# Optimization experiments

Hardware: AMD Instinct MI355X
Metric: run time of the kernel (lower is better)

Reference implementation:

```python
import jax, jax.numpy as jnp
import numpy as np

STRIDE = 16
A = 9
PRE_NMS_TOP_N = 6000
POST_NMS_TOP_N = 300
NMS_THRESH = 0.7
MIN_SIZE = 16
H, W = 128, 192


def _generate_anchors(base_size=16, ratios=(0.5, 1.0, 2.0), scales=(8, 16, 32)):
    base = np.array([0, 0, base_size - 1, base_size - 1], dtype=np.float64)
    w = base[2] - base[0] + 1
    h = base[3] - base[1] + 1
    x_ctr = base[0] + 0.5 * (w - 1)
    y_ctr = base[1] + 0.5 * (h - 1)
    size = w * h
    ratios = np.array(ratios)
    ws = np.round(np.sqrt(size / ratios))
    hs = np.round(ws * ratios)
    ratio_anchors = np.stack([x_ctr - 0.5 * (ws - 1), y_ctr - 0.5 * (hs - 1),
                              x_ctr + 0.5 * (ws - 1), y_ctr + 0.5 * (hs - 1)], axis=1)
    out = []
    scales = np.array(scales)
    for a in ratio_anchors:
        aw = a[2] - a[0] + 1
        ah = a[3] - a[1] + 1
        xc = a[0] + 0.5 * (aw - 1)
        yc = a[1] + 0.5 * (ah - 1)
        ws2 = aw * scales
        hs2 = ah * scales
        out.append(np.stack([xc - 0.5 * (ws2 - 1), yc - 0.5 * (hs2 - 1),
                             xc + 0.5 * (ws2 - 1), yc + 0.5 * (hs2 - 1)], axis=1))
    return np.concatenate(out, axis=0).astype(np.float32)  # [9,4]


def setup_inputs() -> dict:
    key = jax.random.key(0)
    k1, k2 = jax.random.split(key)
    scores = jax.random.uniform(k1, (1, 2 * A, H, W), dtype=jnp.float32)
    bbox_deltas = 0.1 * jax.random.normal(k2, (1, 4 * A, H, W), dtype=jnp.float32)
    im_info = jnp.array([[H * STRIDE, W * STRIDE, 1.0]], dtype=jnp.float32)
    return {"scores": scores, "bbox_deltas": bbox_deltas, "im_info": im_info}


def _proposal_forward(scores, bbox_deltas, im_info):
    anchors_base = jnp.asarray(_generate_anchors())  # [A,4]
    sc = scores[:, A:, :, :]                          # fg scores [1,A,H,W]
    h, w = sc.shape[-2], sc.shape[-1]
    shift_x = (jnp.arange(w) * STRIDE).astype(sc.dtype)
    shift_y = (jnp.arange(h) * STRIDE).astype(sc.dtype)
    sy, sx = jnp.meshgrid(shift_y, shift_x, indexing='ij')
    shifts = jnp.stack([sx.ravel(), sy.ravel(), sx.ravel(), sy.ravel()], axis=1)  # [K,4]
    anchors = (anchors_base[None, :, :] + shifts[:, None, :]).reshape(-1, 4)      # [K*A,4]

    deltas = bbox_deltas.transpose(0, 2, 3, 1).reshape(-1, 4)
    deltas = jnp.concatenate([deltas[:, :2], jnp.clip(deltas[:, 2:], -10.0, 10.0)], axis=1)
    sc = sc.transpose(0, 2, 3, 1).reshape(-1)  # [K*A]

    widths = anchors[:, 2] - anchors[:, 0] + 1.0
    heights = anchors[:, 3] - anchors[:, 1] + 1.0
    ctr_x = anchors[:, 0] + 0.5 * widths
    ctr_y = anchors[:, 1] + 0.5 * heights
    dx, dy, dw, dh = deltas[:, 0], deltas[:, 1], deltas[:, 2], deltas[:, 3]
    pcx = dx * widths + ctr_x
    pcy = dy * heights + ctr_y
    pw = jnp.exp(dw) * widths
    ph = jnp.exp(dh) * heights
    x1 = pcx - 0.5 * pw
    y1 = pcy - 0.5 * ph
    x2 = pcx + 0.5 * pw
    y2 = pcy + 0.5 * ph

    info = im_info[0]
    x1 = jnp.clip(x1, 0.0, info[1] - 1.0)
    x2 = jnp.clip(x2, 0.0, info[1] - 1.0)
    y1 = jnp.clip(y1, 0.0, info[0] - 1.0)
    y2 = jnp.clip(y2, 0.0, info[0] - 1.0)
    proposals = jnp.stack([x1, y1, x2, y2], axis=1)

    # filter_boxes: mask (instead of dropping) boxes smaller than min_size*scale
    min_sz = MIN_SIZE * info[2]
    valid = ((x2 - x1 + 1.0) >= min_sz) & ((y2 - y1 + 1.0) >= min_sz)
    masked = jnp.where(valid, sc, -jnp.inf)

    # sort desc + pre_nms_topN
    top_scores, top_idx = jax.lax.top_k(masked, PRE_NMS_TOP_N)
    boxes = proposals[top_idx]               # [PRE,4], score-descending
    tvalid = top_scores > -jnp.inf

    # pairwise IoU (torchvision convention)
    area = (boxes[:, 2] - boxes[:, 0]) * (boxes[:, 3] - boxes[:, 1])
    lt = jnp.maximum(boxes[:, None, :2], boxes[None, :, :2])
    rb = jnp.minimum(boxes[:, None, 2:], boxes[None, :, 2:])
    wh = jnp.clip(rb - lt, 0.0)
    inter = wh[..., 0] * wh[..., 1]
    iou = inter / (area[:, None] + area[None, :] - inter)  # [PRE,PRE]

    # greedy NMS over score-sorted boxes
    n = PRE_NMS_TOP_N
    def step(keep, x):
        iou_col, v, i = x
        suppressed = jnp.any(keep & (iou_col > NMS_THRESH))
        k = v & jnp.logical_not(suppressed)
        keep = keep.at[i].set(k)
        return keep, k
    keep, _ = jax.lax.scan(step, jnp.zeros((n,), dtype=bool),
                           (iou.T, tvalid, jnp.arange(n)))

    # kept boxes first (stable => score order preserved), take post_nms_topN
    order = jnp.argsort(jnp.logical_not(keep).astype(jnp.int32), stable=True)[:POST_NMS_TOP_N]
    kept = keep[order]
    out_boxes = jnp.where(kept[:, None], boxes[order], 0.0)
    output = jnp.concatenate(
        [jnp.zeros((POST_NMS_TOP_N, 1), out_boxes.dtype), out_boxes], axis=1)
    return output  # [POST,5]: (batch_idx=0, x1,y1,x2,y2); rows beyond kept count are zero


def reference(scores, bbox_deltas, im_info):
    return _proposal_forward(scores, bbox_deltas, im_info)
```

## Files before the change

kernel.cpp:

```cpp
#include <hip/hip_runtime.h>

#define N_ANCH 221184
#define HW     24576
#define Wd     192
#define AA     9
#define TOPN   6000
#define POSTN  300
#define NWORDS 94
#define NCHUNK 47
#define GRID   512
#define GSTRIDE (GRID * 256)
#define SEGSZ  1024
#define CAND_CAP 8192

typedef unsigned long long u64;
typedef unsigned int u32;

__device__ const float c_aw[9] = {184.f,368.f,736.f,128.f,256.f,512.f, 88.f,176.f,352.f};
__device__ const float c_ah[9] = { 96.f,192.f,384.f,128.f,256.f,512.f,176.f,352.f,704.f};

__device__ __forceinline__ u32 ald32(const u32* p) {
    return __hip_atomic_load((const u32*)p, __ATOMIC_RELAXED, __HIP_MEMORY_SCOPE_AGENT);
}
__device__ __forceinline__ void ast32(u32* p, u32 v) {
    __hip_atomic_store(p, v, __ATOMIC_RELAXED, __HIP_MEMORY_SCOPE_AGENT);
}
__device__ __forceinline__ u64 ald64(const u64* p) {
    return __hip_atomic_load((const u64*)p, __ATOMIC_RELAXED, __HIP_MEMORY_SCOPE_AGENT);
}
__device__ __forceinline__ void ast64(u64* p, u64 v) {
    __hip_atomic_store(p, v, __ATOMIC_RELAXED, __HIP_MEMORY_SCOPE_AGENT);
}
__device__ __forceinline__ void stf4(float4* p, float4 v) {
    u64 lo, hi;
    float2 a = make_float2(v.x, v.y), b = make_float2(v.z, v.w);
    __builtin_memcpy(&lo, &a, 8); __builtin_memcpy(&hi, &b, 8);
    ast64((u64*)p, lo); ast64(((u64*)p) + 1, hi);
}
__device__ __forceinline__ float4 ldf4(const float4* p) {
    u64 lo = ald64((const u64*)p), hi = ald64(((const u64*)p) + 1);
    float2 a, b;
    __builtin_memcpy(&a, &lo, 8); __builtin_memcpy(&b, &hi, 8);
    return make_float4(a.x, a.y, b.x, b.y);
}

__device__ __forceinline__ void gbar(u32* bar, u32 target) {
    __syncthreads();
    if (threadIdx.x == 0) {
        __hip_atomic_fetch_add(bar, 1u, __ATOMIC_RELAXED, __HIP_MEMORY_SCOPE_AGENT);
        int guard = 0;
        while (__hip_atomic_load(bar, __ATOMIC_RELAXED, __HIP_MEMORY_SCOPE_AGENT) < target) {
            __builtin_amdgcn_s_sleep(1);
            if (++guard > (1 << 22)) break;
        }
    }
    __syncthreads();
}

__device__ __forceinline__ float4 decode_box(int a, int cell,
                                             const float* __restrict__ deltas,
                                             float info0, float info1, float info2,
                                             bool* valid) {
    int h = cell / Wd;
    int w = cell - h * Wd;
    const float* db = deltas + (size_t)(4 * a) * HW + cell;
    float dx = db[0];
    float dy = db[HW];
    float dw = db[2 * HW];
    float dh = db[3 * HW];
    dw = fminf(fmaxf(dw, -10.f), 10.f);
    dh = fminf(fmaxf(dh, -10.f), 10.f);

    float ww = c_aw[a], hh = c_ah[a];
    float cx = 16.f * (float)w + 8.f;
    float cy = 16.f * (float)h + 8.f;

    float pcx = __fadd_rn(__fmul_rn(dx, ww), cx);
    float pcy = __fadd_rn(__fmul_rn(dy, hh), cy);
    float pw  = __fmul_rn(expf(dw), ww);
    float ph  = __fmul_rn(expf(dh), hh);
    float hpw = __fmul_rn(0.5f, pw);
    float hph = __fmul_rn(0.5f, ph);
    float x1 = __fsub_rn(pcx, hpw);
    float x2 = __fadd_rn(pcx, hpw);
    float y1 = __fsub_rn(pcy, hph);
    float y2 = __fadd_rn(pcy, hph);

    float xmax = __fsub_rn(info1, 1.f);
    float ymax = __fsub_rn(info0, 1.f);
    x1 = fminf(fmaxf(x1, 0.f), xmax);
    x2 = fminf(fmaxf(x2, 0.f), xmax);
    y1 = fminf(fmaxf(y1, 0.f), ymax);
    y2 = fminf(fmaxf(y2, 0.f), ymax);

    float msz = __fmul_rn(16.f, info2);
    *valid = (__fadd_rn(__fsub_rn(x2, x1), 1.f) >= msz) &&
             (__fadd_rn(__fsub_rn(y2, y1), 1.f) >= msz);
    return make_float4(x1, y1, x2, y2);
}

__device__ __forceinline__ u64 rdl64(u64 v, int l) {
    u32 lo = (u32)__builtin_amdgcn_readlane((int)(u32)v, l);
    u32 hi = (u32)__builtin_amdgcn_readlane((int)(u32)(v >> 32), l);
    return ((u64)hi << 32) | (u64)lo;
}

__global__ __launch_bounds__(256, 2) void fused_kernel(
        const float* __restrict__ scores, const float* __restrict__ deltas,
        const float* __restrict__ iminfo, float* __restrict__ out,
        u32* __restrict__ bar, u32* __restrict__ hist1, u32* __restrict__ hist2,
        u32* __restrict__ segctr, u64* __restrict__ vmask,
        u32* __restrict__ keys, u64* __restrict__ cand,
        float4* __restrict__ tb, u64* __restrict__ mat) {
    int tid = threadIdx.x;
    int bid = blockIdx.x;
    int lane = tid & 63;
    int wv = tid >> 6;

    __shared__ u32 lh[256];
    __shared__ u32 sfx[256];
    __shared__ u32 h2w[4][256];
    __shared__ u64 stage[2048];
    __shared__ float4 cbw[4][64];
    __shared__ int kept[POSTN];
    __shared__ u32 sP, sRank, sT;

    float info0 = iminfo[0], info1 = iminfo[1], info2 = iminfo[2];

    lh[tid] = 0u;
    __syncthreads();
    #pragma unroll
    for (int j = 0; j < 2; ++j) {
        int t = j * GSTRIDE + bid * 256 + tid;
        if (t < N_ANCH) {
            int a = t / HW;
            int cell = t - a * HW;
            float score = scores[(AA + a) * HW + cell];
            bool valid;
            (void)decode_box(a, cell, deltas, info0, info1, info2, &valid);
            u32 sb = __float_as_uint(score);
            u32 key = valid ? ((sb & 0x80000000u) ? ~sb : (sb | 0x80000000u))
                            : 0x007FFFFFu;
            ast32(&keys[t], key);
            atomicAdd(&lh[key >> 24], 1u);
        }
    }
    __syncthreads();
    if (lh[tid]) atomicAdd(&hist1[tid], lh[tid]);
    gbar(bar, 1 * GRID);

    sfx[tid] = ald32(&hist1[tid]);
    __syncthreads();
    for (int d = 1; d < 256; d <<= 1) {
        u32 v = (tid + d < 256) ? sfx[tid + d] : 0u;
        __syncthreads();
        sfx[tid] += v;
        __syncthreads();
    }
    {
        u32 ge = sfx[tid];
        u32 gt = (tid < 255) ? sfx[tid + 1] : 0u;
        if (ge >= TOPN && gt < TOPN) { sP = (u32)tid; sRank = TOPN - gt; }
    }
    for (int i = tid; i < 4 * 256; i += 256) ((u32*)h2w)[i] = 0u;
    __syncthreads();
    u32 P = sP, rankP = sRank;
    #pragma unroll
    for (int j = 0; j < 2; ++j) {
        int t = j * GSTRIDE + bid * 256 + tid;
        if (t < N_ANCH) {
            u32 k = ald32(&keys[t]);
            if ((k >> 24) == P) atomicAdd(&h2w[wv][(k >> 16) & 0xFFu], 1u);
        }
    }
    __syncthreads();
    {
        u32 s4 = h2w[0][tid] + h2w[1][tid] + h2w[2][tid] + h2w[3][tid];
        if (s4) atomicAdd(&hist2[tid], s4);
    }
    gbar(bar, 2 * GRID);

    sfx[tid] = ald32(&hist2[tid]);
    __syncthreads();
    for (int d = 1; d < 256; d <<= 1) {
        u32 v = (tid + d < 256) ? sfx[tid + d] : 0u;
        __syncthreads();
        sfx[tid] += v;
        __syncthreads();
    }
    {
        u32 ge = sfx[tid];
        u32 gt = (tid < 255) ? sfx[tid + 1] : 0u;
        if (ge >= rankP && gt < rankP) sT = (P << 24) | ((u32)tid << 16);
    }
    __syncthreads();
    u32 T = sT;
    #pragma unroll
    for (int j = 0; j < 2; ++j) {
        int t = j * GSTRIDE + bid * 256 + tid;
        if (t < N_ANCH) {
            u32 k = ald32(&keys[t]);
            if (k >= T) {
                int seg = bid & 7;
                u32 pos = atomicAdd(&segctr[32 * seg], 1u);
                if (pos < SEGSZ) {
                    int a = t / HW;
                    int cell = t - a * HW;
                    u32 aidx = (u32)(cell * 9 + a);
                    ast64(&cand[seg * SEGSZ + pos], ((u64)k << 32) | (u64)(~aidx));
                }
            }
        }
    }
    gbar(bar, 3 * GRID);

    {
        u32 cc[8];
        #pragma unroll
        for (int s = 0; s < 8; ++s) {
            cc[s] = ald32(&segctr[32 * s]);
            if (cc[s] > SEGSZ) cc[s] = SEGSZ;
        }
        int part = tid & 15;
        int i = bid * 16 + (tid >> 4);
        int iseg = i >> 10, ioff = i & 1023;
        bool active = (u32)ioff < cc[iseg];
        u64 k = active ? ald64(&cand[i]) : 0ull;
        u32 cnt = 0;
        for (int q = 0; q < 4; ++q) {
            for (int j = tid; j < 2048; j += 256) {
                int g = q * 2048 + j;
                int s_ = g >> 10, off = g & 1023;
                stage[j] = ((u32)off < cc[s_]) ? ald64(&cand[g]) : 0ull;
            }
            __syncthreads();
            const ulonglong2* sv = (const ulonglong2*)stage;
            for (int jj = part; jj < 1024; jj += 16) {
                ulonglong2 v = sv[jj];
                cnt += (v.x > k) ? 1u : 0u;
                cnt += (v.y > k) ? 1u : 0u;
            }
            __syncthreads();
        }
        cnt += __shfl_xor(cnt, 1);
        cnt += __shfl_xor(cnt, 2);
        cnt += __shfl_xor(cnt, 4);
        cnt += __shfl_xor(cnt, 8);
        if (part == 0 && active && cnt < TOPN) {
            u32 aidx = ~((u32)k);
            int a = (int)(aidx % 9u);
            int cell = (int)(aidx / 9u);
            bool valid;
            float4 box = decode_box(a, cell, deltas, info0, info1, info2, &valid);
            stf4(&tb[cnt], box);
            if ((u32)(k >> 32) != 0x007FFFFFu)
                atomicOr(&vmask[cnt >> 6], 1ull << (cnt & 63));
        }
    }
    gbar(bar, 4 * GRID);

    {
        int waveid = bid * 4 + wv;
        for (int j = waveid; j < 94 * 94; j += GRID * 4) {
            int by = j / 94;
            int bx = j - by * 94;
            if (bx < by) continue;
            int c0 = bx * 64;
            {
                int col = c0 + lane;
                cbw[wv][lane] = (col < TOPN) ? ldf4(&tb[col]) : make_float4(0.f, 0.f, 0.f, 0.f);
            }
            int row = by * 64 + lane;
            if (row < TOPN) {
                float4 rb = ldf4(&tb[row]);
                float rA = (rb.z - rb.x) * (rb.w - rb.y);
                u64 mask = 0ull;
                for (int c = 0; c < 64; ++c) {
                    if (c0 + c >= TOPN) break;
                    float4 b = cbw[wv][c];
                    float lx = fmaxf(rb.x, b.x), ly = fmaxf(rb.y, b.y);
                    float rx = fminf(rb.z, b.z), ry = fminf(rb.w, b.w);
                    float iw = fmaxf(rx - lx, 0.f), ih = fmaxf(ry - ly, 0.f);
                    float inter = iw * ih;
                    float bA = (b.z - b.x) * (b.w - b.y);
                    float iou = inter / ((rA + bA) - inter);
                    if (iou > 0.7f) mask |= (1ull << c);
                }
                ast64(&mat[(size_t)row * NWORDS + bx], mask);
            }
        }
    }
    gbar(bar, 5 * GRID);

    if (bid == 0 && tid < 64) {
        u64 r0 = ~ald64(&vmask[lane]);
        u64 r1 = (lane < NWORDS - 64) ? ~ald64(&vmask[64 + lane]) : ~0ull;
        int cnt = 0;
        for (int c = 0; c < NCHUNK; ++c) {
            int w2 = 2 * c;
            u64 s0 = (w2 < 64) ? rdl64(r0, w2) : rdl64(r1, w2 - 64);
            u64 s1 = (w2 + 1 < 64) ? rdl64(r0, w2 + 1) : rdl64(r1, w2 + 1 - 64);
            if ((s0 & s1) == ~0ull) continue;
            int base = c * 128;
            const u64* rowA = mat + (size_t)(base + lane) * NWORDS + w2;
            const u64* rowB = mat + (size_t)(base + 64 + lane) * NWORDS + w2;
            u64 ax = ald64(rowA), ay = ald64(rowA + 1);
            u64 bx_ = ald64(rowB), by_ = ald64(rowB + 1);
            u64 rem0 = s0, rem1 = s1, k0 = 0ull, k1 = 0ull;
            while (cnt < POSTN) {
                int b;
                if (~rem0) b = __ffsll((u64)~rem0) - 1;
                else if (~rem1) b = 64 + __ffsll((u64)~rem1) - 1;
                else break;
                if (lane == 0) kept[cnt] = base + b;
                ++cnt;
                if (b < 64) {
                    rem0 |= rdl64(ax, b) | (1ull << b);
                    rem1 |= rdl64(ay, b);
                    k0 |= 1ull << b;
                } else {
                    int bb = b - 64;
                    rem0 |= rdl64(bx_, bb);
                    rem1 |= rdl64(by_, bb) | (1ull << bb);
                    k1 |= 1ull << bb;
                }
            }
            if (cnt >= POSTN) break;
            u64 f0 = 0ull, f1 = 0ull, m0 = k0, m1 = k1;
            while (m0 | m1) {
                int idx[16];
                #pragma unroll
                for (int j = 0; j < 16; ++j) {
                    int b = -1;
                    if (m0) { b = __ffsll(m0) - 1; m0 &= m0 - 1; }
                    else if (m1) { b = 64 + __ffsll(m1) - 1; m1 &= m1 - 1; }
                    idx[j] = b;
                }
                u64 v0[16], v1[16];
                #pragma unroll
                for (int j = 0; j < 16; ++j) {
                    v0[j] = 0ull; v1[j] = 0ull;
                    if (idx[j] >= 0) {
                        const u64* row = mat + (size_t)(base + idx[j]) * NWORDS;
                        v0[j] = ald64(row + lane);
                        if (lane < NWORDS - 64) v1[j] = ald64(row + 64 + lane);
                    }
                }
                #pragma unroll
                for (int j = 0; j < 16; ++j) { f0 |= v0[j]; f1 |= v1[j]; }
            }
            r0 |= f0; r1 |= f1;
        }
        for (int r = lane; r < POSTN; r += 64) {
            float4 b2 = make_float4(0.f, 0.f, 0.f, 0.f);
            if (r < cnt) b2 = ldf4(&tb[kept[r]]);
            float* o = out + r * 5;
            o[0] = 0.f; o[1] = b2.x; o[2] = b2.y; o[3] = b2.z; o[4] = b2.w;
        }
    }
}

extern "C" void kernel_launch(void* const* d_in, const int* in_sizes, int n_in,
                              void* d_out, int out_size, void* d_ws, size_t ws_size,
                              hipStream_t stream) {
    const float* scores = (const float*)d_in[0];
    const float* deltas = (const float*)d_in[1];
    const float* iminfo = (const float*)d_in[2];
    float* out = (float*)d_out;

    char* ws = (char*)d_ws;
    u32* bar    = (u32*)(ws + 0);
    u32* hist1  = (u32*)(ws + 64);
    u32* hist2  = (u32*)(ws + 1088);
    u32* segctr = (u32*)(ws + 2112);
    u64* vmask  = (u64*)(ws + 4160);
    u32* keys   = (u32*)(ws + 8192);
    u64* cand   = (u64*)(ws + 892928);
    float4* tb  = (float4*)(ws + 958464);
    u64* mat    = (u64*)(ws + 1054720);

    hipMemsetAsync(ws, 0, 8192, stream);
    fused_kernel<<<GRID, 256, 0, stream>>>(scores, deltas, iminfo, out,
                                           bar, hist1, hist2, segctr, vmask,
                                           keys, cand, tb, mat);
}
```

Baseline: 276.2 us.

## Widen NMS scan chunks to 256 with prefetched diagonal blocks and flag barrier

Result: faster. 261.9 us (-5.2%).

```diff
diff --git a/kernel.cpp b/kernel.cpp
--- a/kernel.cpp
+++ b/kernel.cpp
@@ -7,9 +7,10 @@
 #define TOPN   6000
 #define POSTN  300
 #define NWORDS 94
-#define NCHUNK 47
+#define NW2    96
+#define NCHUNK 24
 #define GRID   512
-#define GSTRIDE (GRID * 256)
+#define PERBLK 432
 #define SEGSZ  1024
 #define CAND_CAP 8192
 
@@ -20,13 +21,13 @@
 __device__ const float c_ah[9] = { 96.f,192.f,384.f,128.f,256.f,512.f,176.f,352.f,704.f};
 
 __device__ __forceinline__ u32 ald32(const u32* p) {
-    return __hip_atomic_load((const u32*)p, __ATOMIC_RELAXED, __HIP_MEMORY_SCOPE_AGENT);
+    return __hip_atomic_load(p, __ATOMIC_RELAXED, __HIP_MEMORY_SCOPE_AGENT);
 }
 __device__ __forceinline__ void ast32(u32* p, u32 v) {
     __hip_atomic_store(p, v, __ATOMIC_RELAXED, __HIP_MEMORY_SCOPE_AGENT);
 }
 __device__ __forceinline__ u64 ald64(const u64* p) {
-    return __hip_atomic_load((const u64*)p, __ATOMIC_RELAXED, __HIP_MEMORY_SCOPE_AGENT);
+    return __hip_atomic_load(p, __ATOMIC_RELAXED, __HIP_MEMORY_SCOPE_AGENT);
 }
 __device__ __forceinline__ void ast64(u64* p, u64 v) {
     __hip_atomic_store(p, v, __ATOMIC_RELAXED, __HIP_MEMORY_SCOPE_AGENT);
@@ -44,14 +45,18 @@
     return make_float4(a.x, a.y, b.x, b.y);
 }
 
-__device__ __forceinline__ void gbar(u32* bar, u32 target) {
+__device__ __forceinline__ void gbar(u32* cnt, u32* flag, u32 epoch) {
     __syncthreads();
     if (threadIdx.x == 0) {
-        __hip_atomic_fetch_add(bar, 1u, __ATOMIC_RELAXED, __HIP_MEMORY_SCOPE_AGENT);
-        int guard = 0;
-        while (__hip_atomic_load(bar, __ATOMIC_RELAXED, __HIP_MEMORY_SCOPE_AGENT) < target) {
-            __builtin_amdgcn_s_sleep(1);
-            if (++guard > (1 << 22)) break;
+        u32 old = __hip_atomic_fetch_add(cnt, 1u, __ATOMIC_RELAXED, __HIP_MEMORY_SCOPE_AGENT);
+        if (old == epoch * GRID - 1u) {
+            ast32(flag, epoch);
+        } else {
+            int guard = 0;
+            while (ald32(flag) < epoch) {
+                __builtin_amdgcn_s_sleep(1);
+                if (++guard > (1 << 22)) break;
+            }
         }
     }
     __syncthreads();
@@ -108,7 +113,8 @@
 __global__ __launch_bounds__(256, 2) void fused_kernel(
         const float* __restrict__ scores, const float* __restrict__ deltas,
         const float* __restrict__ iminfo, float* __restrict__ out,
-        u32* __restrict__ bar, u32* __restrict__ hist1, u32* __restrict__ hist2,
+        u32* __restrict__ bar, u32* __restrict__ flag,
+        u32* __restrict__ hist1, u32* __restrict__ hist2,
         u32* __restrict__ segctr, u64* __restrict__ vmask,
         u32* __restrict__ keys, u64* __restrict__ cand,
         float4* __restrict__ tb, u64* __restrict__ mat) {
@@ -126,13 +132,15 @@
     __shared__ u32 sP, sRank, sT;
 
     float info0 = iminfo[0], info1 = iminfo[1], info2 = iminfo[2];
+    int tbase = bid * PERBLK;
 
     lh[tid] = 0u;
     __syncthreads();
     #pragma unroll
     for (int j = 0; j < 2; ++j) {
-        int t = j * GSTRIDE + bid * 256 + tid;
-        if (t < N_ANCH) {
+        int i = j * 256 + tid;
+        if (i < PERBLK) {
+            int t = tbase + i;
             int a = t / HW;
             int cell = t - a * HW;
             float score = scores[(AA + a) * HW + cell];
@@ -147,7 +155,7 @@
     }
     __syncthreads();
     if (lh[tid]) atomicAdd(&hist1[tid], lh[tid]);
-    gbar(bar, 1 * GRID);
+    gbar(bar, flag, 1);
 
     sfx[tid] = ald32(&hist1[tid]);
     __syncthreads();
@@ -167,9 +175,9 @@
     u32 P = sP, rankP = sRank;
     #pragma unroll
     for (int j = 0; j < 2; ++j) {
-        int t = j * GSTRIDE + bid * 256 + tid;
-        if (t < N_ANCH) {
-            u32 k = ald32(&keys[t]);
+        int i = j * 256 + tid;
+        if (i < PERBLK) {
+            u32 k = ald32(&keys[tbase + i]);
             if ((k >> 24) == P) atomicAdd(&h2w[wv][(k >> 16) & 0xFFu], 1u);
         }
     }
@@ -178,7 +186,7 @@
         u32 s4 = h2w[0][tid] + h2w[1][tid] + h2w[2][tid] + h2w[3][tid];
         if (s4) atomicAdd(&hist2[tid], s4);
     }
-    gbar(bar, 2 * GRID);
+    gbar(bar, flag, 2);
 
     sfx[tid] = ald32(&hist2[tid]);
     __syncthreads();
@@ -197,8 +205,9 @@
     u32 T = sT;
     #pragma unroll
     for (int j = 0; j < 2; ++j) {
-        int t = j * GSTRIDE + bid * 256 + tid;
-        if (t < N_ANCH) {
+        int i = j * 256 + tid;
+        if (i < PERBLK) {
+            int t = tbase + i;
             u32 k = ald32(&keys[t]);
             if (k >= T) {
                 int seg = bid & 7;
@@ -212,7 +221,7 @@
             }
         }
     }
-    gbar(bar, 3 * GRID);
+    gbar(bar, flag, 3);
 
     {
         u32 cc[8];
@@ -257,7 +266,7 @@
                 atomicOr(&vmask[cnt >> 6], 1ull << (cnt & 63));
         }
     }
-    gbar(bar, 4 * GRID);
+    gbar(bar, flag, 4);
 
     {
         int waveid = bid * 4 + wv;
@@ -286,70 +295,100 @@
                     float iou = inter / ((rA + bA) - inter);
                     if (iou > 0.7f) mask |= (1ull << c);
                 }
-                ast64(&mat[(size_t)row * NWORDS + bx], mask);
-            }
-        }
-    }
-    gbar(bar, 5 * GRID);
+                ast64(&mat[(size_t)row * NW2 + bx], mask);
+            }
+        }
+    }
+    gbar(bar, flag, 5);
 
     if (bid == 0 && tid < 64) {
         u64 r0 = ~ald64(&vmask[lane]);
         u64 r1 = (lane < NWORDS - 64) ? ~ald64(&vmask[64 + lane]) : ~0ull;
         int cnt = 0;
+        u64 dg[4][4];
+        #pragma unroll
+        for (int q = 0; q < 4; ++q) {
+            const u64* rp = mat + (size_t)(q * 64 + lane) * NW2;
+            dg[q][0] = ald64(rp); dg[q][1] = ald64(rp + 1);
+            dg[q][2] = ald64(rp + 2); dg[q][3] = ald64(rp + 3);
+        }
         for (int c = 0; c < NCHUNK; ++c) {
-            int w2 = 2 * c;
-            u64 s0 = (w2 < 64) ? rdl64(r0, w2) : rdl64(r1, w2 - 64);
-            u64 s1 = (w2 + 1 < 64) ? rdl64(r0, w2 + 1) : rdl64(r1, w2 + 1 - 64);
-            if ((s0 & s1) == ~0ull) continue;
-            int base = c * 128;
-            const u64* rowA = mat + (size_t)(base + lane) * NWORDS + w2;
-            const u64* rowB = mat + (size_t)(base + 64 + lane) * NWORDS + w2;
-            u64 ax = ald64(rowA), ay = ald64(rowA + 1);
-            u64 bx_ = ald64(rowB), by_ = ald64(rowB + 1);
-            u64 rem0 = s0, rem1 = s1, k0 = 0ull, k1 = 0ull;
-            while (cnt < POSTN) {
-                int b;
-                if (~rem0) b = __ffsll((u64)~rem0) - 1;
-                else if (~rem1) b = 64 + __ffsll((u64)~rem1) - 1;
-                else break;
-                if (lane == 0) kept[cnt] = base + b;
-                ++cnt;
-                if (b < 64) {
-                    rem0 |= rdl64(ax, b) | (1ull << b);
-                    rem1 |= rdl64(ay, b);
-                    k0 |= 1ull << b;
-                } else {
-                    int bb = b - 64;
-                    rem0 |= rdl64(bx_, bb);
-                    rem1 |= rdl64(by_, bb) | (1ull << bb);
-                    k1 |= 1ull << bb;
+            u64 nd[4][4];
+            #pragma unroll
+            for (int q = 0; q < 4; ++q) { nd[q][0]=0; nd[q][1]=0; nd[q][2]=0; nd[q][3]=0; }
+            if (c + 1 < NCHUNK) {
+                int nb = (c + 1) * 256, nw = 4 * (c + 1);
+                #pragma unroll
+                for (int q = 0; q < 4; ++q) {
+                    const u64* rp = mat + (size_t)(nb + q * 64 + lane) * NW2 + nw;
+                    nd[q][0] = ald64(rp); nd[q][1] = ald64(rp + 1);
+                    nd[q][2] = ald64(rp + 2); nd[q][3] = ald64(rp + 3);
                 }
             }
-            if (cnt >= POSTN) break;
-            u64 f0 = 0ull, f1 = 0ull, m0 = k0, m1 = k1;
-            while (m0 | m1) {
-                int idx[16];
-                #pragma unroll
-                for (int j = 0; j < 16; ++j) {
-                    int b = -1;
-                    if (m0) { b = __ffsll(m0) - 1; m0 &= m0 - 1; }
-                    else if (m1) { b = 64 + __ffsll(m1) - 1; m1 &= m1 - 1; }
-                    idx[j] = b;
+            int w0 = 4 * c;
+            u64 s0 = (w0     < 64) ? rdl64(r0, w0)     : rdl64(r1, w0 - 64);
+            u64 s1 = (w0 + 1 < 64) ? rdl64(r0, w0 + 1) : rdl64(r1, w0 - 63);
+            u64 s2 = (w0 + 2 < 64) ? rdl64(r0, w0 + 2) : rdl64(r1, w0 - 62);
+            u64 s3 = (w0 + 3 < 64) ? rdl64(r0, w0 + 3) : rdl64(r1, w0 - 61);
+            if ((s0 & s1 & s2 & s3) != ~0ull) {
+                int base = c * 256;
+                u64 rem0 = s0, rem1 = s1, rem2 = s2, rem3 = s3;
+                u64 km0 = 0, km1 = 0, km2 = 0, km3 = 0;
+                while (cnt < POSTN) {
+                    int b;
+                    if (~rem0) b = __ffsll((u64)~rem0) - 1;
+                    else if (~rem1) b = 64  + __ffsll((u64)~rem1) - 1;
+                    else if (~rem2) b = 128 + __ffsll((u64)~rem2) - 1;
+                    else if (~rem3) b = 192 + __ffsll((u64)~rem3) - 1;
+                    else break;
+                    if (lane == 0) kept[cnt] = base + b;
+                    ++cnt;
+                    int q = b >> 6, l = b & 63;
+                    u64 v0, v1, v2, v3;
+                    if (q == 0)      { v0=dg[0][0]; v1=dg[0][1]; v2=dg[0][2]; v3=dg[0][3]; }
+                    else if (q == 1) { v0=dg[1][0]; v1=dg[1][1]; v2=dg[1][2]; v3=dg[1][3]; }
+                    else if (q == 2) { v0=dg[2][0]; v1=dg[2][1]; v2=dg[2][2]; v3=dg[2][3]; }
+                    else             { v0=dg[3][0]; v1=dg[3][1]; v2=dg[3][2]; v3=dg[3][3]; }
+                    rem0 |= rdl64(v0, l); rem1 |= rdl64(v1, l);
+                    rem2 |= rdl64(v2, l); rem3 |= rdl64(v3, l);
+                    u64 bit = 1ull << l;
+                    if (q == 0)      { rem0 |= bit; km0 |= bit; }
+                    else if (q == 1) { rem1 |= bit; km1 |= bit; }
+                    else if (q == 2) { rem2 |= bit; km2 |= bit; }
+                    else             { rem3 |= bit; km3 |= bit; }
                 }
-                u64 v0[16], v1[16];
-                #pragma unroll
-                for (int j = 0; j < 16; ++j) {
-                    v0[j] = 0ull; v1[j] = 0ull;
-                    if (idx[j] >= 0) {
-                        const u64* row = mat + (size_t)(base + idx[j]) * NWORDS;
-                        v0[j] = ald64(row + lane);
-                        if (lane < NWORDS - 64) v1[j] = ald64(row + 64 + lane);
+                if (cnt >= POSTN) break;
+                u64 f0 = 0ull, f1 = 0ull;
+                while (km0 | km1 | km2 | km3) {
+                    int idx[16];
+                    #pragma unroll
+                    for (int j = 0; j < 16; ++j) {
+                        int b = -1;
+                        if (km0)      { b = __ffsll(km0) - 1;        km0 &= km0 - 1; }
+                        else if (km1) { b = 64  + __ffsll(km1) - 1;  km1 &= km1 - 1; }
+                        else if (km2) { b = 128 + __ffsll(km2) - 1;  km2 &= km2 - 1; }
+                        else if (km3) { b = 192 + __ffsll(km3) - 1;  km3 &= km3 - 1; }
+                        idx[j] = b;
                     }
+                    u64 a0[16], a1[16];
+                    #pragma unroll
+                    for (int j = 0; j < 16; ++j) {
+                        a0[j] = 0ull; a1[j] = 0ull;
+                        if (idx[j] >= 0) {
+                            const u64* row = mat + (size_t)(base + idx[j]) * NW2;
+                            a0[j] = ald64(row + lane);
+                            if (lane < NWORDS - 64) a1[j] = ald64(row + 64 + lane);
+                        }
+                    }
+                    #pragma unroll
+                    for (int j = 0; j < 16; ++j) { f0 |= a0[j]; f1 |= a1[j]; }
                 }
-                #pragma unroll
-                for (int j = 0; j < 16; ++j) { f0 |= v0[j]; f1 |= v1[j]; }
-            }
-            r0 |= f0; r1 |= f1;
+                r0 |= f0; r1 |= f1;
+            }
+            #pragma unroll
+            for (int q = 0; q < 4; ++q) {
+                dg[q][0]=nd[q][0]; dg[q][1]=nd[q][1]; dg[q][2]=nd[q][2]; dg[q][3]=nd[q][3];
+            }
         }
         for (int r = lane; r < POSTN; r += 64) {
             float4 b2 = make_float4(0.f, 0.f, 0.f, 0.f);
@@ -370,10 +409,11 @@
 
     char* ws = (char*)d_ws;
     u32* bar    = (u32*)(ws + 0);
-    u32* hist1  = (u32*)(ws + 64);
-    u32* hist2  = (u32*)(ws + 1088);
-    u32* segctr = (u32*)(ws + 2112);
-    u64* vmask  = (u64*)(ws + 4160);
+    u32* flag   = (u32*)(ws + 128);
+    u32* hist1  = (u32*)(ws + 256);
+    u32* hist2  = (u32*)(ws + 1280);
+    u32* segctr = (u32*)(ws + 2304);
+    u64* vmask  = (u64*)(ws + 3328);
     u32* keys   = (u32*)(ws + 8192);
     u64* cand   = (u64*)(ws + 892928);
     float4* tb  = (float4*)(ws + 958464);
@@ -381,6 +421,6 @@
 
     hipMemsetAsync(ws, 0, 8192, stream);
     fused_kernel<<<GRID, 256, 0, stream>>>(scores, deltas, iminfo, out,
-                                           bar, hist1, hist2, segctr, vmask,
+                                           bar, flag, hist1, hist2, segctr, vmask,
                                            keys, cand, tb, mat);
 }
```
